# Kernel tuning notes

Measured on AMD Instinct MI355X. Metric: run time of the kernel, lower is better.

Reference implementation:

```python
import jax, jax.numpy as jnp
import numpy as np

B, LQ, LK = 4, 512, 512
QS, KS, H, DV = 512, 512, 256, 512


def setup_inputs() -> dict:
    key = jax.random.key(0)
    ks = jax.random.split(key, 9)
    s_q = 1.0 / np.sqrt(QS)
    s_k = 1.0 / np.sqrt(KS)
    s_v = 1.0 / np.sqrt(H)
    return {
        "query": jax.random.normal(ks[0], (B, LQ, QS), jnp.float32),
        "key": jax.random.normal(ks[1], (B, LK, KS), jnp.float32),
        "value": jax.random.normal(ks[2], (B, LK, DV), jnp.float32),
        "wq": jax.random.uniform(ks[3], (H, QS), jnp.float32, -s_q, s_q),
        "bq": jax.random.uniform(ks[4], (H,), jnp.float32, -s_q, s_q),
        "wk": jax.random.uniform(ks[5], (H, KS), jnp.float32, -s_k, s_k),
        "bk": jax.random.uniform(ks[6], (H,), jnp.float32, -s_k, s_k),
        "wv": jax.random.uniform(ks[7], (H,), jnp.float32, -s_v, s_v),
        "bv": jax.random.uniform(ks[8], (), jnp.float32, -s_v, s_v),
    }


def reference(query, key, value, wq, bq, wk, bk, wv, bv):
    # q: [B, Lq, H], k: [B, Lk, H]
    q = jnp.einsum('bqd,hd->bqh', query, wq) + bq
    k = jnp.einsum('bkd,hd->bkh', key, wk) + bk
    # broadcast add -> [B, Lq, Lk, H], tanh, project to scalar score
    feats = jnp.tanh(q[:, :, None, :] + k[:, None, :, :])
    scores = jnp.einsum('bqkh,h->bqk', feats, wv) + bv  # [B, Lq, Lk]
    attn = jax.nn.softmax(scores, axis=-1)
    # dropout p=0.0 (identity at inference)
    return jnp.einsum('bqk,bkd->bqd', attn, value)
```

## Files before the change

kernel.cpp:

```cpp
#include <hip/hip_runtime.h>

#define LOG2E 1.4426950408889634f

constexpr int Bb = 4, LQ = 512, LK = 512, QS = 512, H = 256, DV = 512;
constexpr int M = 2048;

constexpr size_t OFF_EQT = 0;
constexpr size_t OFF_EKT = 2u << 20;
constexpr size_t OFF_PQ  = 4u << 20;
constexpr size_t OFF_ROW = 6u << 20;

using bf16x8 = __attribute__((ext_vector_type(8))) short;
using f32x4v = __attribute__((ext_vector_type(4))) float;

__device__ inline unsigned short f2bf(float x) {
    unsigned int u = __float_as_uint(x);
    u += 0x7FFFu + ((u >> 16) & 1u);
    return (unsigned short)(u >> 16);
}
__device__ inline unsigned int pk2(float lo, float hi) {
    return (unsigned int)f2bf(lo) | ((unsigned int)f2bf(hi) << 16);
}

__global__ __launch_bounds__(256) void proj_mfma(
    const float* __restrict__ query, const float* __restrict__ key,
    const float* __restrict__ wq, const float* __restrict__ wk,
    const float* __restrict__ bq, const float* __restrict__ bk,
    char* __restrict__ ws, float scale)
{
    const int z = blockIdx.z;
    const float* A    = z ? key : query;
    const float* W    = z ? wk : wq;
    const float* bias = z ? bk : bq;
    float* out = (float*)(ws + (z ? OFF_EKT : OFF_EQT));

    __shared__ unsigned short Als[64][136];
    __shared__ unsigned short Wls[64][136];
    __shared__ float Ot[64][68];

    const int mb = blockIdx.x * 64, nb = blockIdx.y * 64;
    const int tid = threadIdx.x;
    const int wid = tid >> 6, lane = tid & 63;
    const int ml = lane & 15, quad = lane >> 4;

    f32x4v acc[4] = {{0,0,0,0},{0,0,0,0},{0,0,0,0},{0,0,0,0}};

    for (int kc = 0; kc < QS; kc += 128) {
        __syncthreads();
#pragma unroll
        for (int it = 0; it < 4; ++it) {
            int u = tid + it * 256;
            int row = u >> 4, c8 = (u & 15) * 8;
            float4 a0 = *(const float4*)(A + (size_t)(mb + row) * 512 + kc + c8);
            float4 a1 = *(const float4*)(A + (size_t)(mb + row) * 512 + kc + c8 + 4);
            uint4 pa = { pk2(a0.x, a0.y), pk2(a0.z, a0.w), pk2(a1.x, a1.y), pk2(a1.z, a1.w) };
            *(uint4*)&Als[row][c8] = pa;
            float4 w0 = *(const float4*)(W + (size_t)(nb + row) * 512 + kc + c8);
            float4 w1 = *(const float4*)(W + (size_t)(nb + row) * 512 + kc + c8 + 4);
            uint4 pw = { pk2(w0.x, w0.y), pk2(w0.z, w0.w), pk2(w1.x, w1.y), pk2(w1.z, w1.w) };
            *(uint4*)&Wls[row][c8] = pw;
        }
        __syncthreads();
#pragma unroll
        for (int s = 0; s < 4; ++s) {
            int k = s * 32 + quad * 8;
            bf16x8 af = *(const bf16x8*)&Als[wid * 16 + ml][k];
#pragma unroll
            for (int nt = 0; nt < 4; ++nt) {
                bf16x8 bfr = *(const bf16x8*)&Wls[nt * 16 + ml][k];
                acc[nt] = __builtin_amdgcn_mfma_f32_16x16x32_bf16(af, bfr, acc[nt], 0, 0, 0);
            }
        }
    }
    __syncthreads();
#pragma unroll
    for (int nt = 0; nt < 4; ++nt)
#pragma unroll
        for (int r = 0; r < 4; ++r)
            Ot[nt * 16 + ml][wid * 16 + quad * 4 + r] = acc[nt][r];
    __syncthreads();
    {
        int r0 = tid >> 2;
        int c0 = (tid & 3) * 16;
        float bs = bias[nb + r0];
#pragma unroll
        for (int g = 0; g < 4; ++g) {
            float4 v = *(const float4*)&Ot[r0][c0 + g * 4];
            float4 o;
            o.x = __builtin_amdgcn_exp2f(fminf(fmaxf(scale * (v.x + bs), -30.f), 30.f));
            o.y = __builtin_amdgcn_exp2f(fminf(fmaxf(scale * (v.y + bs), -30.f), 30.f));
            o.z = __builtin_amdgcn_exp2f(fminf(fmaxf(scale * (v.z + bs), -30.f), 30.f));
            o.w = __builtin_amdgcn_exp2f(fminf(fmaxf(scale * (v.w + bs), -30.f), 30.f));
            *(float4*)(out + (size_t)(nb + r0) * 2048 + mb + c0 + g * 4) = o;
        }
    }
}

__global__ __launch_bounds__(256) void score_kernel(
    const float* __restrict__ wvp, char* __restrict__ ws)
{
    const float* EqT = (const float*)(ws + OFF_EQT);
    const float* EkT = (const float*)(ws + OFF_EKT);
    unsigned short* Pq = (unsigned short*)(ws + OFF_PQ);
    float* rowpart = (float*)(ws + OFF_ROW);

    __shared__ float Qs[64][64];
    __shared__ float Ks[64][64];
    __shared__ float Wv2[H];
    __shared__ float redS[4][64];

    const int b  = blockIdx.z;
    const int qb = blockIdx.x * 64;
    const int kt = blockIdx.y;
    const int kb = kt * 64;
    const int tid = threadIdx.x;
    const int tx = tid & 15;
    const int ty = tid >> 4;
    const int w  = tid >> 6;
    const int lane = tid & 63;

    Wv2[tid] = wvp[tid] * (2.0f * LOG2E);

    const int mq = b * LQ + qb;
    const int mk = b * LK + kb;
    const int sh = tid >> 4;
    const int sm = (tid & 15) * 4;

    float acc[4][4] = {};

    for (int h0 = 0; h0 < H; h0 += 64) {
        __syncthreads();
#pragma unroll
        for (int it = 0; it < 4; ++it) {
            int h = sh + 16 * it;
            *(float4*)&Qs[h][sm] = *(const float4*)(EqT + (size_t)(h0 + h) * M + mq + sm);
            *(float4*)&Ks[h][sm] = *(const float4*)(EkT + (size_t)(h0 + h) * M + mk + sm);
        }
        __syncthreads();
#pragma unroll 4
        for (int hh = 0; hh < 64; hh += 2) {
            float4 q1 = *(const float4*)&Qs[hh][tx * 4];
            float4 q2 = *(const float4*)&Qs[hh + 1][tx * 4];
            float4 k1 = *(const float4*)&Ks[hh][ty * 4];
            float4 k2 = *(const float4*)&Ks[hh + 1][ty * 4];
            float w1 = Wv2[h0 + hh];
            float w2 = Wv2[h0 + hh + 1];
            const float q1a[4] = {q1.x, q1.y, q1.z, q1.w};
            const float q2a[4] = {q2.x, q2.y, q2.z, q2.w};
            const float k1a[4] = {k1.x, k1.y, k1.z, k1.w};
            const float k2a[4] = {k2.x, k2.y, k2.z, k2.w};
#pragma unroll
            for (int i = 0; i < 4; ++i)
#pragma unroll
                for (int j = 0; j < 4; ++j) {
                    float ta = fmaf(q1a[i], k1a[j], 1.0f);
                    float tb = fmaf(q2a[i], k2a[j], 1.0f);
                    float num = fmaf(w1, tb, w2 * ta);
                    acc[i][j] = fmaf(num, __builtin_amdgcn_rcpf(ta * tb), acc[i][j]);
                }
        }
    }

    float ps[4];
#pragma unroll
    for (int i = 0; i < 4; ++i) {
        int q = qb + tx * 4 + i;
        float p0 = __builtin_amdgcn_exp2f(-acc[i][0]);
        float p1 = __builtin_amdgcn_exp2f(-acc[i][1]);
        float p2 = __builtin_amdgcn_exp2f(-acc[i][2]);
        float p3 = __builtin_amdgcn_exp2f(-acc[i][3]);
        ps[i] = (p0 + p1) + (p2 + p3);
        uint2 o = { pk2(p0, p1), pk2(p2, p3) };
        *(uint2*)(Pq + ((size_t)(b * 512 + q) * 512 + kb + ty * 4)) = o;
    }
#pragma unroll
    for (int i = 0; i < 4; ++i) {
        ps[i] += __shfl_xor(ps[i], 16, 64);
        ps[i] += __shfl_xor(ps[i], 32, 64);
    }
    if (lane < 16) {
#pragma unroll
        for (int i = 0; i < 4; ++i) redS[w][tx * 4 + i] = ps[i];
    }
    __syncthreads();
    if (tid < 64) {
        float s = (redS[0][tid] + redS[1][tid]) + (redS[2][tid] + redS[3][tid]);
        rowpart[(size_t)kt * 2048 + b * 512 + qb + tid] = s;
    }
}

__global__ __launch_bounds__(256) void av_mfma(
    const float* __restrict__ V, const char* __restrict__ wsc,
    float* __restrict__ O)
{
    const unsigned short* Pq = (const unsigned short*)(wsc + OFF_PQ);
    const float* rowpart = (const float*)(wsc + OFF_ROW);

    __shared__ unsigned short Pls[64][136];
    __shared__ unsigned short Vls[64][136];

    const int b = blockIdx.z, qb = blockIdx.x * 64, nb = blockIdx.y * 64;
    const int tid = threadIdx.x;
    const int wid = tid >> 6, lane = tid & 63;
    const int ml = lane & 15, quad = lane >> 4;
    const unsigned short* Pb = Pq + (size_t)b * 512 * 512;
    const float* Vb = V + (size_t)b * 512 * 512;

    f32x4v acc[4] = {{0,0,0,0},{0,0,0,0},{0,0,0,0},{0,0,0,0}};

    for (int kc = 0; kc < LK; kc += 128) {
        __syncthreads();
#pragma unroll
        for (int it = 0; it < 4; ++it) {
            int u = tid + it * 256;
            int row = u >> 4, c8 = (u & 15) * 8;
            *(uint4*)&Pls[row][c8] = *(const uint4*)(Pb + (size_t)(qb + row) * 512 + kc + c8);
        }
#pragma unroll
        for (int it = 0; it < 8; ++it) {
            int u = tid + it * 256;
            int k = u >> 4, c4 = (u & 15) * 4;
            float4 v4 = *(const float4*)(Vb + (size_t)(kc + k) * 512 + nb + c4);
            Vls[c4 + 0][k] = f2bf(v4.x);
            Vls[c4 + 1][k] = f2bf(v4.y);
            Vls[c4 + 2][k] = f2bf(v4.z);
            Vls[c4 + 3][k] = f2bf(v4.w);
        }
        __syncthreads();
#pragma unroll
        for (int s = 0; s < 4; ++s) {
            int k = s * 32 + quad * 8;
            bf16x8 af = *(const bf16x8*)&Pls[wid * 16 + ml][k];
#pragma unroll
            for (int nt = 0; nt < 4; ++nt) {
                bf16x8 bfr = *(const bf16x8*)&Vls[nt * 16 + ml][k];
                acc[nt] = __builtin_amdgcn_mfma_f32_16x16x32_bf16(af, bfr, acc[nt], 0, 0, 0);
            }
        }
    }

    float rr[4];
#pragma unroll
    for (int r = 0; r < 4; ++r) {
        int q = qb + wid * 16 + quad * 4 + r;
        float rs = 0.f;
#pragma unroll
        for (int t = 0; t < 8; ++t) rs += rowpart[(size_t)t * 2048 + b * 512 + q];
        rr[r] = 1.0f / rs;
    }
#pragma unroll
    for (int nt = 0; nt < 4; ++nt)
#pragma unroll
        for (int r = 0; r < 4; ++r) {
            int q = qb + wid * 16 + quad * 4 + r;
            O[((size_t)b * 512 + q) * 512 + nb + nt * 16 + ml] = acc[nt][r] * rr[r];
        }
}

extern "C" void kernel_launch(void* const* d_in, const int* in_sizes, int n_in,
                              void* d_out, int out_size, void* d_ws, size_t ws_size,
                              hipStream_t stream) {
    const float* query = (const float*)d_in[0];
    const float* key   = (const float*)d_in[1];
    const float* value = (const float*)d_in[2];
    const float* wq    = (const float*)d_in[3];
    const float* bq    = (const float*)d_in[4];
    const float* wk    = (const float*)d_in[5];
    const float* bk    = (const float*)d_in[6];
    const float* wv    = (const float*)d_in[7];
    float* out = (float*)d_out;
    char* ws = (char*)d_ws;

    const float c2 = 2.0f * LOG2E;

    proj_mfma<<<dim3(32, 4, 2), 256, 0, stream>>>(query, key, wq, wk, bq, bk, ws, c2);
    score_kernel<<<dim3(8, 8, Bb), 256, 0, stream>>>(wv, ws);
    av_mfma<<<dim3(8, 8, Bb), 256, 0, stream>>>(value, ws, out);
}
```

Before: 140.3 us.

## Prefetch next H-chunk into registers and double-buffer LDS operand reads

The next 64-row slices of EqT/EkT are now loaded from global memory into registers while the current chunk is being computed from LDS, hiding global load latency behind the tanh-score arithmetic. The inner loop also loads the next iteration's q/k float4 values from shared memory ahead of use (software pipelining of LDS reads). This costs extra VGPRs for the prefetch buffers and the next operands, which may reduce occupancy. The wrap-around read at the last step of each chunk is redundant but harmless.

```diff
diff --git a/kernel.cpp b/kernel.cpp
--- a/kernel.cpp
+++ b/kernel.cpp
@@ -126,25 +126,43 @@
     const int sh = tid >> 4;
     const int sm = (tid & 15) * 4;
 
+    float4 pq[4], pk[4];
+#pragma unroll
+    for (int it = 0; it < 4; ++it) {
+        pq[it] = *(const float4*)(EqT + (size_t)(sh + 16 * it) * M + mq + sm);
+        pk[it] = *(const float4*)(EkT + (size_t)(sh + 16 * it) * M + mk + sm);
+    }
+
     float acc[4][4] = {};
 
     for (int h0 = 0; h0 < H; h0 += 64) {
         __syncthreads();
 #pragma unroll
         for (int it = 0; it < 4; ++it) {
-            int h = sh + 16 * it;
-            *(float4*)&Qs[h][sm] = *(const float4*)(EqT + (size_t)(h0 + h) * M + mq + sm);
-            *(float4*)&Ks[h][sm] = *(const float4*)(EkT + (size_t)(h0 + h) * M + mk + sm);
-        }
-        __syncthreads();
+            *(float4*)&Qs[sh + 16 * it][sm] = pq[it];
+            *(float4*)&Ks[sh + 16 * it][sm] = pk[it];
+        }
+        __syncthreads();
+        if (h0 + 64 < H) {
+#pragma unroll
+            for (int it = 0; it < 4; ++it) {
+                pq[it] = *(const float4*)(EqT + (size_t)(h0 + 64 + sh + 16 * it) * M + mq + sm);
+                pk[it] = *(const float4*)(EkT + (size_t)(h0 + 64 + sh + 16 * it) * M + mk + sm);
+            }
+        }
+        float4 q1 = *(const float4*)&Qs[0][tx * 4];
+        float4 q2 = *(const float4*)&Qs[1][tx * 4];
+        float4 k1 = *(const float4*)&Ks[0][ty * 4];
+        float4 k2 = *(const float4*)&Ks[1][ty * 4];
 #pragma unroll 4
         for (int hh = 0; hh < 64; hh += 2) {
-            float4 q1 = *(const float4*)&Qs[hh][tx * 4];
-            float4 q2 = *(const float4*)&Qs[hh + 1][tx * 4];
-            float4 k1 = *(const float4*)&Ks[hh][ty * 4];
-            float4 k2 = *(const float4*)&Ks[hh + 1][ty * 4];
-            float w1 = Wv2[h0 + hh];
-            float w2 = Wv2[h0 + hh + 1];
+            const int hn = (hh + 2) & 63;
+            float4 q1n = *(const float4*)&Qs[hn][tx * 4];
+            float4 q2n = *(const float4*)&Qs[hn + 1][tx * 4];
+            float4 k1n = *(const float4*)&Ks[hn][ty * 4];
+            float4 k2n = *(const float4*)&Ks[hn + 1][ty * 4];
+            const float w1 = Wv2[h0 + hh];
+            const float w2 = Wv2[h0 + hh + 1];
             const float q1a[4] = {q1.x, q1.y, q1.z, q1.w};
             const float q2a[4] = {q2.x, q2.y, q2.z, q2.w};
             const float k1a[4] = {k1.x, k1.y, k1.z, k1.w};
@@ -158,6 +176,7 @@
                     float num = fmaf(w1, tb, w2 * ta);
                     acc[i][j] = fmaf(num, __builtin_amdgcn_rcpf(ta * tb), acc[i][j]);
                 }
+            q1 = q1n; q2 = q2n; k1 = k1n; k2 = k2n;
         }
     }
 
```

Result: slower. 149.3 us (+6.4%).
